# Optimization experiments

Measured on AMD Instinct MI355X. Metric: run time of the kernel, lower is better.

## Reference

```python
import jax, jax.numpy as jnp
import numpy as np

HIDDEN = 1024
HEADS = 16
HEAD_DIM = HIDDEN // HEADS
SEQ = 2048
BATCH = 2


def setup_inputs() -> dict:
    key = jax.random.key(0)
    ks = jax.random.split(key, 11)
    s = 1.0 / np.sqrt(HIDDEN)
    inp = {
        'query': jax.random.normal(ks[0], (SEQ, BATCH, HIDDEN), jnp.float32),
        'key': jax.random.normal(ks[1], (SEQ, BATCH, HIDDEN), jnp.float32),
        'value': jax.random.normal(ks[2], (SEQ, BATCH, HIDDEN), jnp.float32),
        'Wq': jax.random.normal(ks[3], (HIDDEN, HIDDEN), jnp.float32) * s,
        'bq': jnp.zeros((HIDDEN,), jnp.float32),
        'Wk': jax.random.normal(ks[4], (HIDDEN, HIDDEN), jnp.float32) * s,
        'bk': jnp.zeros((HIDDEN,), jnp.float32),
        'Wv': jax.random.normal(ks[5], (HIDDEN, HIDDEN), jnp.float32) * s,
        'bv': jnp.zeros((HIDDEN,), jnp.float32),
        'Wo': jax.random.normal(ks[6], (HIDDEN, HIDDEN), jnp.float32) * s,
        'bo': jnp.zeros((HIDDEN,), jnp.float32),
    }
    return inp


def reference(query, key, value, Wq, bq, Wk, bk, Wv, bv, Wo, bo):
    # Linear layers: torch Linear computes x @ W.T + b
    S, B, _ = query.shape
    q = (query @ Wq.T + bq).reshape(S, B, HEADS, HEAD_DIM)
    k = (key @ Wk.T + bk).reshape(S, B, HEADS, HEAD_DIM)
    v = (value @ Wv.T + bv).reshape(S, B, HEADS, HEAD_DIM)
    # -> [B, H, S, D]
    q = jnp.transpose(q, (1, 2, 0, 3))
    k = jnp.transpose(k, (1, 2, 0, 3))
    v = jnp.transpose(v, (1, 2, 0, 3))
    scores = jnp.einsum('bhqd,bhkd->bhqk', q, k) / np.sqrt(HEAD_DIM)
    attn = jax.nn.softmax(scores, axis=-1)  # dropout=0.0 -> identity
    out = jnp.einsum('bhqk,bhkd->bhqd', attn, v)
    out = jnp.transpose(out, (2, 0, 1, 3)).reshape(S, B, HIDDEN)
    out = out @ Wo.T + bo
    return out, attn
```

## Files before the change

### kernel.cpp

```cpp
#include <hip/hip_runtime.h>
#include <hip/hip_bf16.h>
#include <cstdint>
#include <cstddef>

#define SEQLEN 2048
#define NBATCH 2
#define NHEAD  16
#define HDIM   64
#define HID    1024
#define MROWS  4096

typedef __bf16 bf16x8 __attribute__((ext_vector_type(8)));
typedef float f32x4 __attribute__((ext_vector_type(4)));
typedef unsigned short ushort8 __attribute__((ext_vector_type(8)));

#define MFMA16(a, b, c) __builtin_amdgcn_mfma_f32_16x16x32_bf16((a), (b), (c), 0, 0, 0)

#define GLOAD_LDS16(g, l)                                                        \
    __builtin_amdgcn_global_load_lds(                                            \
        (const __attribute__((address_space(1))) void*)(g),                      \
        (__attribute__((address_space(3))) void*)(l), 16, 0, 0)

__global__ __launch_bounds__(256) void qkv_proj(
    const float* __restrict__ xq, const float* __restrict__ xk, const float* __restrict__ xv,
    const float* __restrict__ Wq, const float* __restrict__ Wk, const float* __restrict__ Wv,
    const float* __restrict__ bq, const float* __restrict__ bk, const float* __restrict__ bv,
    unsigned short* __restrict__ Qb, unsigned short* __restrict__ Kb, unsigned short* __restrict__ Vb)
{
    const int z = blockIdx.z;
    const float* X    = (z == 0) ? xq : (z == 1) ? xk : xv;
    const float* W    = (z == 0) ? Wq : (z == 1) ? Wk : Wv;
    const float* bias = (z == 0) ? bq : (z == 1) ? bk : bv;
    unsigned short* dst = (z == 0) ? Qb : (z == 1) ? Kb : Vb;

    __shared__ unsigned short Ah[128][40];
    __shared__ unsigned short Bh[128][40];

    const int t = threadIdx.x;
    const int lane = t & 63, wid = t >> 6;
    const int wm = wid >> 1, wn = wid & 1;
    const int bm = blockIdx.x * 128, bn = blockIdx.y * 128;
    const int srow = t >> 1, scol = (t & 1) * 16;
    const int fr = lane & 15, fk = (lane >> 4) * 8;

    f32x4 acc[4][4] = {};

    for (int k0 = 0; k0 < HID; k0 += 32) {
        __syncthreads();
        {
            const float4* src = (const float4*)(X + (size_t)(bm + srow) * HID + k0 + scol);
            float4 f0 = src[0], f1 = src[1], f2 = src[2], f3 = src[3];
            float xs[16] = {f0.x, f0.y, f0.z, f0.w, f1.x, f1.y, f1.z, f1.w,
                            f2.x, f2.y, f2.z, f2.w, f3.x, f3.y, f3.z, f3.w};
            bf16x8 h0, h1;
            #pragma unroll
            for (int j = 0; j < 8; ++j) { h0[j] = (__bf16)xs[j]; h1[j] = (__bf16)xs[j + 8]; }
            *(bf16x8*)&Ah[srow][scol]     = h0;
            *(bf16x8*)&Ah[srow][scol + 8] = h1;
        }
        {
            const float4* src = (const float4*)(W + (size_t)(bn + srow) * HID + k0 + scol);
            float4 f0 = src[0], f1 = src[1], f2 = src[2], f3 = src[3];
            float xs[16] = {f0.x, f0.y, f0.z, f0.w, f1.x, f1.y, f1.z, f1.w,
                            f2.x, f2.y, f2.z, f2.w, f3.x, f3.y, f3.z, f3.w};
            bf16x8 h0, h1;
            #pragma unroll
            for (int j = 0; j < 8; ++j) { h0[j] = (__bf16)xs[j]; h1[j] = (__bf16)xs[j + 8]; }
            *(bf16x8*)&Bh[srow][scol]     = h0;
            *(bf16x8*)&Bh[srow][scol + 8] = h1;
        }
        __syncthreads();

        bf16x8 a_h[4], b_h[4];
        #pragma unroll
        for (int m = 0; m < 4; ++m) a_h[m] = *(const bf16x8*)&Ah[wm * 64 + m * 16 + fr][fk];
        #pragma unroll
        for (int n = 0; n < 4; ++n) b_h[n] = *(const bf16x8*)&Bh[wn * 64 + n * 16 + fr][fk];
        #pragma unroll
        for (int m = 0; m < 4; ++m)
            #pragma unroll
            for (int n = 0; n < 4; ++n)
                acc[m][n] = MFMA16(a_h[m], b_h[n], acc[m][n]);
    }

    const int fg = lane >> 4;
    #pragma unroll
    for (int n = 0; n < 4; ++n) {
        const int gc = bn + wn * 64 + n * 16 + fr;
        const float bb = bias[gc];
        #pragma unroll
        for (int m = 0; m < 4; ++m)
            #pragma unroll
            for (int r = 0; r < 4; ++r) {
                const int gr = bm + wm * 64 + m * 16 + fg * 4 + r;
                *(__bf16*)&dst[(size_t)gr * HID + gc] = (__bf16)(acc[m][n][r] + bb);
            }
    }
}

__global__ __launch_bounds__(256) void vtrans(
    const unsigned short* __restrict__ Vb, unsigned short* __restrict__ Vt)
{
    const int t = threadIdx.x;
    const int s = blockIdx.x * 256 + t;
    const int h = blockIdx.y, b = blockIdx.z;

    const unsigned short* src = Vb + ((size_t)s * 2 + b) * HID + h * HDIM;
    ushort8 v[8];
    #pragma unroll
    for (int i = 0; i < 8; ++i) v[i] = *(const ushort8*)(src + i * 8);

    unsigned short* dst = Vt + (((size_t)(b * NHEAD + h)) << 17) + s;
    #pragma unroll
    for (int i = 0; i < 8; ++i)
        #pragma unroll
        for (int j = 0; j < 8; ++j)
            dst[(size_t)(i * 8 + j) * SEQLEN] = v[i][j];
}

__global__ __launch_bounds__(256) void attn2(
    const unsigned short* __restrict__ Qb, const unsigned short* __restrict__ Kb,
    const unsigned short* __restrict__ Vt, float* __restrict__ attn_out,
    unsigned short* __restrict__ Hb)
{
    __shared__ unsigned short Ks[128 * 64];
    __shared__ unsigned short Pl[4 * 32 * 128];

    const int flat = blockIdx.x + (blockIdx.y << 4) + (blockIdx.z << 8);
    const int nf = (flat & 7) * 64 + (flat >> 3);
    const int qblk = nf & 15, h = (nf >> 4) & 15, b = nf >> 8;

    const int t = threadIdx.x, lane = t & 63, w = t >> 6;
    const int fr = lane & 15, fg = lane >> 4;
    const int fg4 = fg << 2, fg16 = fg << 4;
    const int qbase = qblk * 128 + w * 32;
    const float scale = 0.125f;

    bf16x8 qf[2][2];
    #pragma unroll
    for (int mi = 0; mi < 2; ++mi) {
        const int q = qbase + mi * 16 + fr;
        const unsigned short* qp = Qb + (((size_t)q * 2 + b) << 10) + (h << 6);
        qf[mi][0] = *(const bf16x8*)(qp + (fg << 3));
        qf[mi][1] = *(const bf16x8*)(qp + 32 + (fg << 3));
    }

    const char* Ksc = (const char*)Ks;
    char* Plc = (char*)&Pl[w * 4096];

    float lsum[2][4] = {};

    for (int kt = 0; kt < 16; ++kt) {
        __syncthreads();
        #pragma unroll
        for (int c = 0; c < 4; ++c) {
            const int row_l = (w << 5) + (c << 3) + (lane >> 3);
            const int sp = (kt << 7) + row_l;
            const unsigned short* src = Kb + (((size_t)sp * 2 + b) << 10) + (h << 6)
                                         + (((lane & 7) ^ (row_l & 7)) << 3);
            GLOAD_LDS16(src, &Ks[((w << 5) + (c << 3)) * 64]);
        }
        __syncthreads();

        f32x4 s_[2][8] = {};
        #pragma unroll
        for (int n = 0; n < 8; ++n) {
            const int row = (n << 4) + fr;
            const int rx = (row & 7) << 4;
            #pragma unroll
            for (int kk = 0; kk < 2; ++kk) {
                bf16x8 kf = *(const bf16x8*)(Ksc + (row << 7) + (((kk << 6) | fg16) ^ rx));
                s_[0][n] = MFMA16(qf[0][kk], kf, s_[0][n]);
                s_[1][n] = MFMA16(qf[1][kk], kf, s_[1][n]);
            }
        }
        #pragma unroll
        for (int mi = 0; mi < 2; ++mi)
            #pragma unroll
            for (int r = 0; r < 4; ++r) {
                float a = 0.f;
                #pragma unroll
                for (int n = 0; n < 8; ++n)
                    a += __expf(fminf(s_[mi][n][r] * scale, 60.f));
                lsum[mi][r] += a;
            }
    }

    float inv[2][4];
    #pragma unroll
    for (int mi = 0; mi < 2; ++mi)
        #pragma unroll
        for (int r = 0; r < 4; ++r) {
            float v = lsum[mi][r];
            v += __shfl_xor(v, 1); v += __shfl_xor(v, 2);
            v += __shfl_xor(v, 4); v += __shfl_xor(v, 8);
            inv[mi][r] = 1.f / v;
        }

    f32x4 oacc[2][4] = {};
    float* attnB = attn_out + ((size_t)((b << 4) + h) << 22);
    const size_t vhead = (size_t)((b << 4) + h) << 6;

    for (int kt = 0; kt < 16; ++kt) {
        __syncthreads();
        #pragma unroll
        for (int c = 0; c < 4; ++c) {
            const int row_l = (w << 5) + (c << 3) + (lane >> 3);
            const int sp = (kt << 7) + row_l;
            const unsigned short* src = Kb + (((size_t)sp * 2 + b) << 10) + (h << 6)
                                         + (((lane & 7) ^ (row_l & 7)) << 3);
            GLOAD_LDS16(src, &Ks[((w << 5) + (c << 3)) * 64]);
        }
        __syncthreads();

        f32x4 s_[2][8] = {};
        #pragma unroll
        for (int n = 0; n < 8; ++n) {
            const int row = (n << 4) + fr;
            const int rx = (row & 7) << 4;
            #pragma unroll
            for (int kk = 0; kk < 2; ++kk) {
                bf16x8 kf = *(const bf16x8*)(Ksc + (row << 7) + (((kk << 6) | fg16) ^ rx));
                s_[0][n] = MFMA16(qf[0][kk], kf, s_[0][n]);
                s_[1][n] = MFMA16(qf[1][kk], kf, s_[1][n]);
            }
        }

        #pragma unroll
        for (int mi = 0; mi < 2; ++mi)
            #pragma unroll
            for (int n = 0; n < 8; ++n) {
                const int colb = (n << 5) | (fr << 1);
                #pragma unroll
                for (int r = 0; r < 4; ++r) {
                    const int row = (mi << 4) + fg4 + r;
                    const float p = __expf(fminf(s_[mi][n][r] * scale, 60.f)) * inv[mi][r];
                    *(__bf16*)(Plc + (row << 8) + (colb ^ ((row & 7) << 4))) = (__bf16)p;
                }
            }
        asm volatile("s_waitcnt lgkmcnt(0)" ::: "memory");
        __builtin_amdgcn_sched_barrier(0);

        {
            float* ab = attnB + (size_t)qbase * SEQLEN + (kt << 7) + (lane << 1);
            #pragma unroll
            for (int j = 0; j < 32; ++j) {
                const unsigned int u =
                    *(const unsigned int*)(Plc + (j << 8) + ((lane << 2) ^ ((j & 7) << 4)));
                float2 f;
                f.x = __builtin_bit_cast(float, u << 16);
                f.y = __builtin_bit_cast(float, u & 0xFFFF0000u);
                *(float2*)(ab + (size_t)j * SEQLEN) = f;
            }
        }

        #pragma unroll
        for (int kk2 = 0; kk2 < 4; ++kk2) {
            const int cb = ((kk2 << 6) | fg16) ^ ((fr & 7) << 4);
            bf16x8 pa0 = *(const bf16x8*)(Plc + (fr << 8) + cb);
            bf16x8 pa1 = *(const bf16x8*)(Plc + ((16 + fr) << 8) + cb);
            #pragma unroll
            for (int n2 = 0; n2 < 4; ++n2) {
                bf16x8 vf = *(const bf16x8*)(Vt + ((vhead + (n2 << 4) + fr) << 11)
                                             + (kt << 7) + (kk2 << 5) + (fg << 3));
                oacc[0][n2] = MFMA16(pa0, vf, oacc[0][n2]);
                oacc[1][n2] = MFMA16(pa1, vf, oacc[1][n2]);
            }
        }
    }

    #pragma unroll
    for (int mi = 0; mi < 2; ++mi)
        #pragma unroll
        for (int n2 = 0; n2 < 4; ++n2)
            #pragma unroll
            for (int r = 0; r < 4; ++r) {
                const int q = qbase + (mi << 4) + fg4 + r;
                *(__bf16*)&Hb[(((size_t)q * 2 + b) << 10) + (h << 6) + (n2 << 4) + fr] =
                    (__bf16)oacc[mi][n2][r];
            }
}

__global__ __launch_bounds__(256) void out_proj(
    const unsigned short* __restrict__ Hb, const float* __restrict__ Wo,
    const float* __restrict__ bo, float* __restrict__ out)
{
    __shared__ unsigned short Ah[128 * 32];
    __shared__ unsigned short Bh[128][40];

    const int t = threadIdx.x;
    const int lane = t & 63, wid = t >> 6;
    const int wm = wid >> 1, wn = wid & 1;
    const int bm = blockIdx.x * 128, bn = blockIdx.y * 128;
    const int srow = t >> 1, scol = (t & 1) * 16;
    const int fr = lane & 15, fg = lane >> 4, fk = fg * 8;

    f32x4 acc[4][4] = {};

    for (int k0 = 0; k0 < HID; k0 += 32) {
        __syncthreads();
        #pragma unroll
        for (int c = 0; c < 2; ++c) {
            const int row_l = wid * 32 + c * 16 + (lane >> 2);
            const unsigned short* src = Hb + (size_t)(bm + row_l) * HID + k0 + ((lane & 3) << 3);
            GLOAD_LDS16(src, &Ah[(wid * 32 + c * 16) * 32]);
        }
        {
            const float4* src = (const float4*)(Wo + (size_t)(bn + srow) * HID + k0 + scol);
            float4 f0 = src[0], f1 = src[1], f2 = src[2], f3 = src[3];
            float xs[16] = {f0.x, f0.y, f0.z, f0.w, f1.x, f1.y, f1.z, f1.w,
                            f2.x, f2.y, f2.z, f2.w, f3.x, f3.y, f3.z, f3.w};
            bf16x8 h0, h1;
            #pragma unroll
            for (int j = 0; j < 8; ++j) { h0[j] = (__bf16)xs[j]; h1[j] = (__bf16)xs[j + 8]; }
            *(bf16x8*)&Bh[srow][scol]     = h0;
            *(bf16x8*)&Bh[srow][scol + 8] = h1;
        }
        __syncthreads();

        bf16x8 a_h[4], b_h[4];
        #pragma unroll
        for (int m = 0; m < 4; ++m)
            a_h[m] = *(const bf16x8*)&Ah[(wm * 64 + m * 16 + fr) * 32 + fk];
        #pragma unroll
        for (int n = 0; n < 4; ++n) b_h[n] = *(const bf16x8*)&Bh[wn * 64 + n * 16 + fr][fk];
        #pragma unroll
        for (int m = 0; m < 4; ++m)
            #pragma unroll
            for (int n = 0; n < 4; ++n)
                acc[m][n] = MFMA16(a_h[m], b_h[n], acc[m][n]);
    }

    const int fg2 = lane >> 4;
    #pragma unroll
    for (int n = 0; n < 4; ++n) {
        const int gc = bn + wn * 64 + n * 16 + fr;
        const float bb = bo[gc];
        #pragma unroll
        for (int m = 0; m < 4; ++m)
            #pragma unroll
            for (int r = 0; r < 4; ++r) {
                const int gr = bm + wm * 64 + m * 16 + fg2 * 4 + r;
                out[(size_t)gr * HID + gc] = acc[m][n][r] + bb;
            }
    }
}

extern "C" void kernel_launch(void* const* d_in, const int* in_sizes, int n_in,
                              void* d_out, int out_size, void* d_ws, size_t ws_size,
                              hipStream_t stream)
{
    (void)in_sizes; (void)n_in; (void)out_size;

    const float* query = (const float*)d_in[0];
    const float* key   = (const float*)d_in[1];
    const float* value = (const float*)d_in[2];
    const float* Wq    = (const float*)d_in[3];
    const float* bq    = (const float*)d_in[4];
    const float* Wk    = (const float*)d_in[5];
    const float* bk    = (const float*)d_in[6];
    const float* Wv    = (const float*)d_in[7];
    const float* bv    = (const float*)d_in[8];
    const float* Wo    = (const float*)d_in[9];
    const float* bo    = (const float*)d_in[10];

    float* out0 = (float*)d_out;
    float* attn = out0 + (size_t)MROWS * HID;

    if (ws_size < (size_t)32 * 1024 * 1024) return;
    const size_t nbuf = (size_t)MROWS * HID;
    unsigned short* Qb = (unsigned short*)d_ws;
    unsigned short* Kb = Qb + nbuf;
    unsigned short* Vb = Kb + nbuf;
    unsigned short* Vt = Vb + nbuf;
    unsigned short* Hb = Vb;

    qkv_proj<<<dim3(32, 8, 3), 256, 0, stream>>>(query, key, value, Wq, Wk, Wv,
                                                 bq, bk, bv, Qb, Kb, Vb);
    vtrans<<<dim3(8, NHEAD, NBATCH), 256, 0, stream>>>(Vb, Vt);
    attn2<<<dim3(16, NHEAD, NBATCH), 256, 0, stream>>>(Qb, Kb, Vt, attn, Hb);
    out_proj<<<dim3(32, 8), 256, 0, stream>>>(Hb, Wo, bo, out0);
}
```

Before: 374.6 us.

## Pre-convert inputs to bf16, use async LDS GEMMs, and write attn directly from registers

Result: faster. 326.6 us (-12.8%).

```diff
diff --git a/kernel.cpp b/kernel.cpp
--- a/kernel.cpp
+++ b/kernel.cpp
@@ -21,69 +21,121 @@
         (const __attribute__((address_space(1))) void*)(g),                      \
         (__attribute__((address_space(3))) void*)(l), 16, 0, 0)
 
-__global__ __launch_bounds__(256) void qkv_proj(
-    const float* __restrict__ xq, const float* __restrict__ xk, const float* __restrict__ xv,
-    const float* __restrict__ Wq, const float* __restrict__ Wk, const float* __restrict__ Wv,
+static __device__ __forceinline__ unsigned int pack_bf16_pair(float lo, float hi) {
+    unsigned short a = __builtin_bit_cast(unsigned short, (__bf16)lo);
+    unsigned short b = __builtin_bit_cast(unsigned short, (__bf16)hi);
+    return ((unsigned int)b << 16) | a;
+}
+
+__global__ __launch_bounds__(256) void conv6(
+    const float* __restrict__ s0, const float* __restrict__ s1, const float* __restrict__ s2,
+    const float* __restrict__ s3, const float* __restrict__ s4, const float* __restrict__ s5,
+    unsigned short* __restrict__ Sc)
+{
+    const int y = blockIdx.y;
+    const float* src = (y == 0) ? s0 : (y == 1) ? s1 : (y == 2) ? s2
+                     : (y == 3) ? s3 : (y == 4) ? s4 : s5;
+    const size_t M1 = 1u << 20;
+    unsigned short* dst = (y < 3) ? (Sc + (size_t)y * 4 * M1) : (Sc + 12 * M1 + (size_t)(y - 3) * M1);
+    const size_t n = (y < 3) ? 4 * M1 : M1;
+
+    const size_t i = ((size_t)blockIdx.x * 256 + threadIdx.x) * 8;
+    if (i >= n) return;
+    float4 f0 = *(const float4*)(src + i);
+    float4 f1 = *(const float4*)(src + i + 4);
+    ushort8 o;
+    o[0] = __builtin_bit_cast(unsigned short, (__bf16)f0.x);
+    o[1] = __builtin_bit_cast(unsigned short, (__bf16)f0.y);
+    o[2] = __builtin_bit_cast(unsigned short, (__bf16)f0.z);
+    o[3] = __builtin_bit_cast(unsigned short, (__bf16)f0.w);
+    o[4] = __builtin_bit_cast(unsigned short, (__bf16)f1.x);
+    o[5] = __builtin_bit_cast(unsigned short, (__bf16)f1.y);
+    o[6] = __builtin_bit_cast(unsigned short, (__bf16)f1.z);
+    o[7] = __builtin_bit_cast(unsigned short, (__bf16)f1.w);
+    *(ushort8*)(dst + i) = o;
+}
+
+__global__ __launch_bounds__(256) void wconv(
+    const float* __restrict__ Wo, unsigned short* __restrict__ Wob)
+{
+    const size_t i = ((size_t)blockIdx.x * 256 + threadIdx.x) * 8;
+    float4 f0 = *(const float4*)(Wo + i);
+    float4 f1 = *(const float4*)(Wo + i + 4);
+    ushort8 o;
+    o[0] = __builtin_bit_cast(unsigned short, (__bf16)f0.x);
+    o[1] = __builtin_bit_cast(unsigned short, (__bf16)f0.y);
+    o[2] = __builtin_bit_cast(unsigned short, (__bf16)f0.z);
+    o[3] = __builtin_bit_cast(unsigned short, (__bf16)f0.w);
+    o[4] = __builtin_bit_cast(unsigned short, (__bf16)f1.x);
+    o[5] = __builtin_bit_cast(unsigned short, (__bf16)f1.y);
+    o[6] = __builtin_bit_cast(unsigned short, (__bf16)f1.z);
+    o[7] = __builtin_bit_cast(unsigned short, (__bf16)f1.w);
+    *(ushort8*)(Wob + i) = o;
+}
+
+#define GEMM_STAGE(LDSBUF, SRCP)                                                  \
+    _Pragma("unroll")                                                             \
+    for (int c = 0; c < 4; ++c) {                                                 \
+        const int rb = (w << 5) + (c << 3);                                       \
+        const int row = rb + (lane >> 3);                                         \
+        const unsigned short* src = (SRCP) + (size_t)row * HID + k0               \
+                                  + (((lane & 7) ^ ((lane >> 3) & 7)) << 3);      \
+        GLOAD_LDS16(src, &LDSBUF[rb * 64]);                                       \
+    }
+
+__global__ __launch_bounds__(256) void qkv_gemm(
+    const unsigned short* __restrict__ Sc,
     const float* __restrict__ bq, const float* __restrict__ bk, const float* __restrict__ bv,
     unsigned short* __restrict__ Qb, unsigned short* __restrict__ Kb, unsigned short* __restrict__ Vb)
 {
     const int z = blockIdx.z;
-    const float* X    = (z == 0) ? xq : (z == 1) ? xk : xv;
-    const float* W    = (z == 0) ? Wq : (z == 1) ? Wk : Wv;
+    const size_t M1 = 1u << 20;
+    const unsigned short* A = Sc + (size_t)z * 4 * M1;
+    const unsigned short* B = Sc + 12 * M1 + (size_t)z * M1;
     const float* bias = (z == 0) ? bq : (z == 1) ? bk : bv;
     unsigned short* dst = (z == 0) ? Qb : (z == 1) ? Kb : Vb;
 
-    __shared__ unsigned short Ah[128][40];
-    __shared__ unsigned short Bh[128][40];
-
-    const int t = threadIdx.x;
-    const int lane = t & 63, wid = t >> 6;
-    const int wm = wid >> 1, wn = wid & 1;
+    __shared__ unsigned short As[128 * 64];
+    __shared__ unsigned short Bs[128 * 64];
+
+    const int t = threadIdx.x, lane = t & 63, w = t >> 6;
+    const int wm = w >> 1, wn = w & 1;
     const int bm = blockIdx.x * 128, bn = blockIdx.y * 128;
-    const int srow = t >> 1, scol = (t & 1) * 16;
-    const int fr = lane & 15, fk = (lane >> 4) * 8;
+    const int fr = lane & 15, fg = lane >> 4;
 
     f32x4 acc[4][4] = {};
-
-    for (int k0 = 0; k0 < HID; k0 += 32) {
-        __syncthreads();
-        {
-            const float4* src = (const float4*)(X + (size_t)(bm + srow) * HID + k0 + scol);
-            float4 f0 = src[0], f1 = src[1], f2 = src[2], f3 = src[3];
-            float xs[16] = {f0.x, f0.y, f0.z, f0.w, f1.x, f1.y, f1.z, f1.w,
-                            f2.x, f2.y, f2.z, f2.w, f3.x, f3.y, f3.z, f3.w};
-            bf16x8 h0, h1;
-            #pragma unroll
-            for (int j = 0; j < 8; ++j) { h0[j] = (__bf16)xs[j]; h1[j] = (__bf16)xs[j + 8]; }
-            *(bf16x8*)&Ah[srow][scol]     = h0;
-            *(bf16x8*)&Ah[srow][scol + 8] = h1;
-        }
-        {
-            const float4* src = (const float4*)(W + (size_t)(bn + srow) * HID + k0 + scol);
-            float4 f0 = src[0], f1 = src[1], f2 = src[2], f3 = src[3];
-            float xs[16] = {f0.x, f0.y, f0.z, f0.w, f1.x, f1.y, f1.z, f1.w,
-                            f2.x, f2.y, f2.z, f2.w, f3.x, f3.y, f3.z, f3.w};
-            bf16x8 h0, h1;
-            #pragma unroll
-            for (int j = 0; j < 8; ++j) { h0[j] = (__bf16)xs[j]; h1[j] = (__bf16)xs[j + 8]; }
-            *(bf16x8*)&Bh[srow][scol]     = h0;
-            *(bf16x8*)&Bh[srow][scol + 8] = h1;
-        }
-        __syncthreads();
-
-        bf16x8 a_h[4], b_h[4];
-        #pragma unroll
-        for (int m = 0; m < 4; ++m) a_h[m] = *(const bf16x8*)&Ah[wm * 64 + m * 16 + fr][fk];
-        #pragma unroll
-        for (int n = 0; n < 4; ++n) b_h[n] = *(const bf16x8*)&Bh[wn * 64 + n * 16 + fr][fk];
-        #pragma unroll
-        for (int m = 0; m < 4; ++m)
-            #pragma unroll
-            for (int n = 0; n < 4; ++n)
-                acc[m][n] = MFMA16(a_h[m], b_h[n], acc[m][n]);
-    }
-
-    const int fg = lane >> 4;
+    const char* Ac = (const char*)As;
+    const char* Bc = (const char*)Bs;
+
+    for (int k0 = 0; k0 < HID; k0 += 64) {
+        __syncthreads();
+        GEMM_STAGE(As, A + (size_t)bm * HID)
+        GEMM_STAGE(Bs, B + (size_t)bn * HID)
+        __syncthreads();
+
+        #pragma unroll
+        for (int kk = 0; kk < 2; ++kk) {
+            bf16x8 a_h[4], b_h[4];
+            #pragma unroll
+            for (int m = 0; m < 4; ++m) {
+                const int row = wm * 64 + m * 16 + fr;
+                a_h[m] = *(const bf16x8*)(Ac + (row << 7) + (((kk << 6) | (fg << 4)) ^ ((row & 7) << 4)));
+            }
+            #pragma unroll
+            for (int n = 0; n < 4; ++n) {
+                const int row = wn * 64 + n * 16 + fr;
+                b_h[n] = *(const bf16x8*)(Bc + (row << 7) + (((kk << 6) | (fg << 4)) ^ ((row & 7) << 4)));
+            }
+            __builtin_amdgcn_s_setprio(1);
+            #pragma unroll
+            for (int m = 0; m < 4; ++m)
+                #pragma unroll
+                for (int n = 0; n < 4; ++n)
+                    acc[m][n] = MFMA16(a_h[m], b_h[n], acc[m][n]);
+            __builtin_amdgcn_s_setprio(0);
+        }
+    }
+
     #pragma unroll
     for (int n = 0; n < 4; ++n) {
         const int gc = bn + wn * 64 + n * 16 + fr;
@@ -101,21 +153,26 @@
 __global__ __launch_bounds__(256) void vtrans(
     const unsigned short* __restrict__ Vb, unsigned short* __restrict__ Vt)
 {
+    __shared__ unsigned short T[64][66];
     const int t = threadIdx.x;
-    const int s = blockIdx.x * 256 + t;
-    const int h = blockIdx.y, b = blockIdx.z;
-
-    const unsigned short* src = Vb + ((size_t)s * 2 + b) * HID + h * HDIM;
-    ushort8 v[8];
-    #pragma unroll
-    for (int i = 0; i < 8; ++i) v[i] = *(const ushort8*)(src + i * 8);
-
-    unsigned short* dst = Vt + (((size_t)(b * NHEAD + h)) << 17) + s;
-    #pragma unroll
-    for (int i = 0; i < 8; ++i)
-        #pragma unroll
-        for (int j = 0; j < 8; ++j)
-            dst[(size_t)(i * 8 + j) * SEQLEN] = v[i][j];
+    const int s0 = blockIdx.x * 64, h = blockIdx.y, b = blockIdx.z;
+
+    {
+        const int s_l = t >> 2, d0 = (t & 3) * 16;
+        const unsigned short* src = Vb + (((size_t)(s0 + s_l) * 2 + b) << 10) + (h << 6) + d0;
+        *(ushort8*)&T[s_l][d0]     = *(const ushort8*)src;
+        *(ushort8*)&T[s_l][d0 + 8] = *(const ushort8*)(src + 8);
+    }
+    __syncthreads();
+    {
+        const int d_l = t >> 2, sc = (t & 3) * 16;
+        ushort8 o0, o1;
+        #pragma unroll
+        for (int j = 0; j < 8; ++j) { o0[j] = T[sc + j][d_l]; o1[j] = T[sc + 8 + j][d_l]; }
+        unsigned short* dst = Vt + (((size_t)((b << 4) + h) * 64 + d_l) << 11) + s0 + sc;
+        *(ushort8*)dst       = o0;
+        *(ushort8*)(dst + 8) = o1;
+    }
 }
 
 __global__ __launch_bounds__(256) void attn2(
@@ -148,21 +205,22 @@
     const char* Ksc = (const char*)Ks;
     char* Plc = (char*)&Pl[w * 4096];
 
-    float lsum[2][4] = {};
+    float lsum[2] = {0.f, 0.f};
 
     for (int kt = 0; kt < 16; ++kt) {
         __syncthreads();
         #pragma unroll
         for (int c = 0; c < 4; ++c) {
-            const int row_l = (w << 5) + (c << 3) + (lane >> 3);
-            const int sp = (kt << 7) + row_l;
-            const unsigned short* src = Kb + (((size_t)sp * 2 + b) << 10) + (h << 6)
+            const int rb = (w << 5) + (c << 3);
+            const int row_l = rb + (lane >> 3);
+            const unsigned short* src = Kb + (((size_t)((kt << 7) + row_l) * 2 + b) << 10) + (h << 6)
                                          + (((lane & 7) ^ (row_l & 7)) << 3);
-            GLOAD_LDS16(src, &Ks[((w << 5) + (c << 3)) * 64]);
+            GLOAD_LDS16(src, &Ks[rb * 64]);
         }
         __syncthreads();
 
         f32x4 s_[2][8] = {};
+        __builtin_amdgcn_s_setprio(1);
         #pragma unroll
         for (int n = 0; n < 8; ++n) {
             const int row = (n << 4) + fr;
@@ -170,32 +228,31 @@
             #pragma unroll
             for (int kk = 0; kk < 2; ++kk) {
                 bf16x8 kf = *(const bf16x8*)(Ksc + (row << 7) + (((kk << 6) | fg16) ^ rx));
-                s_[0][n] = MFMA16(qf[0][kk], kf, s_[0][n]);
-                s_[1][n] = MFMA16(qf[1][kk], kf, s_[1][n]);
-            }
-        }
-        #pragma unroll
-        for (int mi = 0; mi < 2; ++mi)
-            #pragma unroll
-            for (int r = 0; r < 4; ++r) {
-                float a = 0.f;
+                s_[0][n] = MFMA16(kf, qf[0][kk], s_[0][n]);
+                s_[1][n] = MFMA16(kf, qf[1][kk], s_[1][n]);
+            }
+        }
+        __builtin_amdgcn_s_setprio(0);
+        #pragma unroll
+        for (int mi = 0; mi < 2; ++mi) {
+            float a = 0.f;
+            #pragma unroll
+            for (int n = 0; n < 8; ++n)
                 #pragma unroll
-                for (int n = 0; n < 8; ++n)
+                for (int r = 0; r < 4; ++r)
                     a += __expf(fminf(s_[mi][n][r] * scale, 60.f));
-                lsum[mi][r] += a;
-            }
-    }
-
-    float inv[2][4];
+            lsum[mi] += a;
+        }
+    }
+
+    float inv[2];
     #pragma unroll
-    for (int mi = 0; mi < 2; ++mi)
-        #pragma unroll
-        for (int r = 0; r < 4; ++r) {
-            float v = lsum[mi][r];
-            v += __shfl_xor(v, 1); v += __shfl_xor(v, 2);
-            v += __shfl_xor(v, 4); v += __shfl_xor(v, 8);
-            inv[mi][r] = 1.f / v;
-        }
+    for (int mi = 0; mi < 2; ++mi) {
+        float v = lsum[mi];
+        v += __shfl_xor(v, 16);
+        v += __shfl_xor(v, 32);
+        inv[mi] = 1.f / v;
+    }
 
     f32x4 oacc[2][4] = {};
     float* attnB = attn_out + ((size_t)((b << 4) + h) << 22);
@@ -205,15 +262,16 @@
         __syncthreads();
         #pragma unroll
         for (int c = 0; c < 4; ++c) {
-            const int row_l = (w << 5) + (c << 3) + (lane >> 3);
-            const int sp = (kt << 7) + row_l;
-            const unsigned short* src = Kb + (((size_t)sp * 2 + b) << 10) + (h << 6)
+            const int rb = (w << 5) + (c << 3);
+            const int row_l = rb + (lane >> 3);
+            const unsigned short* src = Kb + (((size_t)((kt << 7) + row_l) * 2 + b) << 10) + (h << 6)
                                          + (((lane & 7) ^ (row_l & 7)) << 3);
-            GLOAD_LDS16(src, &Ks[((w << 5) + (c << 3)) * 64]);
+            GLOAD_LDS16(src, &Ks[rb * 64]);
         }
         __syncthreads();
 
         f32x4 s_[2][8] = {};
+        __builtin_amdgcn_s_setprio(1);
         #pragma unroll
         for (int n = 0; n < 8; ++n) {
             const int row = (n << 4) + fr;
@@ -221,39 +279,34 @@
             #pragma unroll
             for (int kk = 0; kk < 2; ++kk) {
                 bf16x8 kf = *(const bf16x8*)(Ksc + (row << 7) + (((kk << 6) | fg16) ^ rx));
-                s_[0][n] = MFMA16(qf[0][kk], kf, s_[0][n]);
-                s_[1][n] = MFMA16(qf[1][kk], kf, s_[1][n]);
-            }
-        }
-
-        #pragma unroll
-        for (int mi = 0; mi < 2; ++mi)
+                s_[0][n] = MFMA16(kf, qf[0][kk], s_[0][n]);
+                s_[1][n] = MFMA16(kf, qf[1][kk], s_[1][n]);
+            }
+        }
+        __builtin_amdgcn_s_setprio(0);
+
+        #pragma unroll
+        for (int mi = 0; mi < 2; ++mi) {
+            float* ab = attnB + ((size_t)(qbase + mi * 16 + fr) << 11) + (kt << 7) + fg4;
+            const int row_l = mi * 16 + fr;
+            const int rxl = (row_l & 7) << 4;
             #pragma unroll
             for (int n = 0; n < 8; ++n) {
-                const int colb = (n << 5) | (fr << 1);
+                f32x4 p;
                 #pragma unroll
-                for (int r = 0; r < 4; ++r) {
-                    const int row = (mi << 4) + fg4 + r;
-                    const float p = __expf(fminf(s_[mi][n][r] * scale, 60.f)) * inv[mi][r];
-                    *(__bf16*)(Plc + (row << 8) + (colb ^ ((row & 7) << 4))) = (__bf16)p;
-                }
-            }
+                for (int r = 0; r < 4; ++r)
+                    p[r] = __expf(fminf(s_[mi][n][r] * scale, 60.f)) * inv[mi];
+                *(f32x4*)(ab + (n << 4)) = p;
+                unsigned int lo = pack_bf16_pair(p[0], p[1]);
+                unsigned int hi = pack_bf16_pair(p[2], p[3]);
+                uint2 pk = {lo, hi};
+                *(uint2*)(Plc + (row_l << 8) + (((n << 5) | (fg << 3)) ^ rxl)) = pk;
+            }
+        }
         asm volatile("s_waitcnt lgkmcnt(0)" ::: "memory");
         __builtin_amdgcn_sched_barrier(0);
 
-        {
-            float* ab = attnB + (size_t)qbase * SEQLEN + (kt << 7) + (lane << 1);
-            #pragma unroll
-            for (int j = 0; j < 32; ++j) {
-                const unsigned int u =
-                    *(const unsigned int*)(Plc + (j << 8) + ((lane << 2) ^ ((j & 7) << 4)));
-                float2 f;
-                f.x = __builtin_bit_cast(float, u << 16);
-                f.y = __builtin_bit_cast(float, u & 0xFFFF0000u);
-                *(float2*)(ab + (size_t)j * SEQLEN) = f;
-            }
-        }
-
+        __builtin_amdgcn_s_setprio(1);
         #pragma unroll
         for (int kk2 = 0; kk2 < 4; ++kk2) {
             const int cb = ((kk2 << 6) | fg16) ^ ((fr & 7) << 4);
@@ -267,6 +320,7 @@
                 oacc[1][n2] = MFMA16(pa1, vf, oacc[1][n2]);
             }
         }
+        __builtin_amdgcn_s_setprio(0);
     }
 
     #pragma unroll
@@ -282,56 +336,50 @@
 }
 
 __global__ __launch_bounds__(256) void out_proj(
-    const unsigned short* __restrict__ Hb, const float* __restrict__ Wo,
+    const unsigned short* __restrict__ Hb, const unsigned short* __restrict__ Wob,
     const float* __restrict__ bo, float* __restrict__ out)
 {
-    __shared__ unsigned short Ah[128 * 32];
-    __shared__ unsigned short Bh[128][40];
-
-    const int t = threadIdx.x;
-    const int lane = t & 63, wid = t >> 6;
-    const int wm = wid >> 1, wn = wid & 1;
+    __shared__ unsigned short As[128 * 64];
+    __shared__ unsigned short Bs[128 * 64];
+
+    const int t = threadIdx.x, lane = t & 63, w = t >> 6;
+    const int wm = w >> 1, wn = w & 1;
     const int bm = blockIdx.x * 128, bn = blockIdx.y * 128;
-    const int srow = t >> 1, scol = (t & 1) * 16;
-    const int fr = lane & 15, fg = lane >> 4, fk = fg * 8;
+    const int fr = lane & 15, fg = lane >> 4;
 
     f32x4 acc[4][4] = {};
-
-    for (int k0 = 0; k0 < HID; k0 += 32) {
-        __syncthreads();
-        #pragma unroll
-        for (int c = 0; c < 2; ++c) {
-            const int row_l = wid * 32 + c * 16 + (lane >> 2);
-            const unsigned short* src = Hb + (size_t)(bm + row_l) * HID + k0 + ((lane & 3) << 3);
-            GLOAD_LDS16(src, &Ah[(wid * 32 + c * 16) * 32]);
-        }
-        {
-            const float4* src = (const float4*)(Wo + (size_t)(bn + srow) * HID + k0 + scol);
-            float4 f0 = src[0], f1 = src[1], f2 = src[2], f3 = src[3];
-            float xs[16] = {f0.x, f0.y, f0.z, f0.w, f1.x, f1.y, f1.z, f1.w,
-                            f2.x, f2.y, f2.z, f2.w, f3.x, f3.y, f3.z, f3.w};
-            bf16x8 h0, h1;
-            #pragma unroll
-            for (int j = 0; j < 8; ++j) { h0[j] = (__bf16)xs[j]; h1[j] = (__bf16)xs[j + 8]; }
-            *(bf16x8*)&Bh[srow][scol]     = h0;
-            *(bf16x8*)&Bh[srow][scol + 8] = h1;
-        }
-        __syncthreads();
-
-        bf16x8 a_h[4], b_h[4];
-        #pragma unroll
-        for (int m = 0; m < 4; ++m)
-            a_h[m] = *(const bf16x8*)&Ah[(wm * 64 + m * 16 + fr) * 32 + fk];
-        #pragma unroll
-        for (int n = 0; n < 4; ++n) b_h[n] = *(const bf16x8*)&Bh[wn * 64 + n * 16 + fr][fk];
-        #pragma unroll
-        for (int m = 0; m < 4; ++m)
-            #pragma unroll
-            for (int n = 0; n < 4; ++n)
-                acc[m][n] = MFMA16(a_h[m], b_h[n], acc[m][n]);
-    }
-
-    const int fg2 = lane >> 4;
+    const char* Ac = (const char*)As;
+    const char* Bc = (const char*)Bs;
+
+    for (int k0 = 0; k0 < HID; k0 += 64) {
+        __syncthreads();
+        GEMM_STAGE(As, Hb + (size_t)bm * HID)
+        GEMM_STAGE(Bs, Wob + (size_t)bn * HID)
+        __syncthreads();
+
+        #pragma unroll
+        for (int kk = 0; kk < 2; ++kk) {
+            bf16x8 a_h[4], b_h[4];
+            #pragma unroll
+            for (int m = 0; m < 4; ++m) {
+                const int row = wm * 64 + m * 16 + fr;
+                a_h[m] = *(const bf16x8*)(Ac + (row << 7) + (((kk << 6) | (fg << 4)) ^ ((row & 7) << 4)));
+            }
+            #pragma unroll
+            for (int n = 0; n < 4; ++n) {
+                const int row = wn * 64 + n * 16 + fr;
+                b_h[n] = *(const bf16x8*)(Bc + (row << 7) + (((kk << 6) | (fg << 4)) ^ ((row & 7) << 4)));
+            }
+            __builtin_amdgcn_s_setprio(1);
+            #pragma unroll
+            for (int m = 0; m < 4; ++m)
+                #pragma unroll
+                for (int n = 0; n < 4; ++n)
+                    acc[m][n] = MFMA16(a_h[m], b_h[n], acc[m][n]);
+            __builtin_amdgcn_s_setprio(0);
+        }
+    }
+
     #pragma unroll
     for (int n = 0; n < 4; ++n) {
         const int gc = bn + wn * 64 + n * 16 + fr;
@@ -340,7 +388,7 @@
         for (int m = 0; m < 4; ++m)
             #pragma unroll
             for (int r = 0; r < 4; ++r) {
-                const int gr = bm + wm * 64 + m * 16 + fg2 * 4 + r;
+                const int gr = bm + wm * 64 + m * 16 + fg * 4 + r;
                 out[(size_t)gr * HID + gc] = acc[m][n][r] + bb;
             }
     }
@@ -355,11 +403,8 @@
     const float* query = (const float*)d_in[0];
     const float* key   = (const float*)d_in[1];
     const float* value = (const float*)d_in[2];
-    const float* Wq    = (const float*)d_in[3];
     const float* bq    = (const float*)d_in[4];
-    const float* Wk    = (const float*)d_in[5];
     const float* bk    = (const float*)d_in[6];
-    const float* Wv    = (const float*)d_in[7];
     const float* bv    = (const float*)d_in[8];
     const float* Wo    = (const float*)d_in[9];
     const float* bo    = (const float*)d_in[10];
@@ -374,10 +419,16 @@
     unsigned short* Vb = Kb + nbuf;
     unsigned short* Vt = Vb + nbuf;
     unsigned short* Hb = Vb;
-
-    qkv_proj<<<dim3(32, 8, 3), 256, 0, stream>>>(query, key, value, Wq, Wk, Wv,
-                                                 bq, bk, bv, Qb, Kb, Vb);
-    vtrans<<<dim3(8, NHEAD, NBATCH), 256, 0, stream>>>(Vb, Vt);
+    unsigned short* Wob = Qb;
+
+    unsigned short* Sc = (unsigned short*)attn;
+
+    conv6<<<dim3(2048, 6), 256, 0, stream>>>(query, key, value,
+                                             (const float*)d_in[3], (const float*)d_in[5],
+                                             (const float*)d_in[7], Sc);
+    qkv_gemm<<<dim3(32, 8, 3), 256, 0, stream>>>(Sc, bq, bk, bv, Qb, Kb, Vb);
+    vtrans<<<dim3(32, NHEAD, NBATCH), 256, 0, stream>>>(Vb, Vt);
     attn2<<<dim3(16, NHEAD, NBATCH), 256, 0, stream>>>(Qb, Kb, Vt, attn, Hb);
-    out_proj<<<dim3(32, 8), 256, 0, stream>>>(Hb, Wo, bo, out0);
-}
+    wconv<<<dim3(512), 256, 0, stream>>>(Wo, Wob);
+    out_proj<<<dim3(32, 8), 256, 0, stream>>>(Hb, Wob, bo, out0);
+}
```
